# Kernel tuning notes

Hardware: AMD Instinct MI355X
Metric: run time of the kernel (lower is better)

## Reference

```python
import jax, jax.numpy as jnp
import numpy as np

BINS = 256
MIN_V = -0.25
MAX_V = 1.25
XSIGMA = 1.0 / float(np.sqrt(2.0 * np.pi))
DELTA = (MAX_V - MIN_V) / BINS
SIGMA = DELTA * XSIGMA
# constant prefactor applied once to the joint kernel: delta / (sqrt(2*pi)*sigma)
COEF = float(DELTA / (np.sqrt(2.0 * np.pi) * SIGMA))

B, N = 8, 32768


def setup_inputs() -> dict:
    key = jax.random.key(0)
    k1, k2, k3 = jax.random.split(key, 3)
    x1 = jax.random.uniform(k1, (B, N), dtype=jnp.float32)
    x2 = jax.random.uniform(k2, (B, N), dtype=jnp.float32)
    mask = jax.random.uniform(k3, (B, N), dtype=jnp.float32)
    return {"x1": x1, "x2": x2, "mask": mask}


def reference(x1, x2, mask):
    # bin centers: (bins,)
    centers = MIN_V + DELTA * (jnp.arange(BINS, dtype=x1.dtype) + 0.5)
    inv_s = 1.0 / SIGMA
    # Separable factorization of exp(-0.5*((x1-ci)^2+(x2-cj)^2)/sigma^2):
    # g1: (b, bins, N), g2: (b, bins, N) with mask folded into g2.
    d1 = (x1[:, None, :] - centers[None, :, None]) * inv_s
    d2 = (x2[:, None, :] - centers[None, :, None]) * inv_s
    g1 = jnp.exp(-0.5 * d1 * d1)
    g2 = jnp.exp(-0.5 * d2 * d2) * mask[:, None, :]
    # contract over N via batched matmul -> (b, bins, bins)
    hist = jnp.einsum("bin,bjn->bij", g1, g2)
    return COEF * hist
```

## Files before the change

### kernel.cpp

```cpp
#include <hip/hip_runtime.h>


#define BINS   256
#define NPTS   32768
#define BATCH  8
#define TROWS  8
#define NTILE  (BINS / TROWS)
#define WORDS  64

static constexpr float kInvDelta = 256.0f / 1.5f;
static constexpr float kUAdd     = 0.25f * (256.0f / 1.5f) - 0.5f;
static constexpr float kPi       = 3.14159265358979323846f;
static constexpr float kFix      = 1024.0f;
static constexpr float kInvFix   = 1.0f / 1024.0f;

__global__ __launch_bounds__(1024) void gh_gather(
    const float* __restrict__ x1, const float* __restrict__ x2,
    const float* __restrict__ mask, float* __restrict__ out)
{
    __shared__ unsigned long long tile[2 * TROWS * WORDS];
    const int tid = threadIdx.x;
    const int r0  = blockIdx.x * TROWS;
    const int b   = blockIdx.y;

    tile[tid] = 0ULL;
    __syncthreads();

    const float4* X1 = (const float4*)(x1   + b * NPTS);
    const float4* X2 = (const float4*)(x2   + b * NPTS);
    const float4* M  = (const float4*)(mask + b * NPTS);

#pragma unroll 2
    for (int it = 0; it < NPTS / 4096; ++it) {
        const int n4 = it * 1024 + tid;
        const float4 a4 = X1[n4];
        const float4 b4 = X2[n4];
        const float4 m4 = M[n4];

        const float pv1[4] = {a4.x, a4.y, a4.z, a4.w};
        const float pv2[4] = {b4.x, b4.y, b4.z, b4.w};
        const float pm[4]  = {m4.x, m4.y, m4.z, m4.w};

#pragma unroll
        for (int k = 0; k < 4; ++k) {
            const float u1 = fmaf(pv1[k], kInvDelta, kUAdd);
            const float u2 = fmaf(pv2[k], kInvDelta, kUAdd);
            const float fi = rintf(u1);
            const int   i0 = (int)fi;
            const float t1 = u1 - fi;

            int e = (((int)rintf(u2)) - 1) & ~1;
            e = min(250, max(0, e));
            const int  ph   = (e >> 1) & 1;
            const int  word = e >> 2;
            const float t2  = u2 - (float)e;

            float w1a[3];
#pragma unroll
            for (int a = 0; a < 3; ++a) {
                const float d = t1 - (float)(a - 1);
                w1a[a] = __expf(-kPi * d * d);
            }
            float W2[4];
#pragma unroll
            for (int c = 0; c < 4; ++c) {
                const float d = t2 - (float)c;
                W2[c] = __expf(-kPi * d * d) * (pm[k] * kFix);
            }

            const int rbase = i0 - 1 - r0;
            const int pbase = ph * (TROWS * WORDS) + word;
#pragma unroll
            for (int a = 0; a < 3; ++a) {
                const int r = rbase + a;
                if ((unsigned)r < TROWS) {
                    const float wa = w1a[a];
                    const unsigned f0 = (unsigned)fmaf(wa, W2[0], 0.5f);
                    const unsigned f1 = (unsigned)fmaf(wa, W2[1], 0.5f);
                    const unsigned f2 = (unsigned)fmaf(wa, W2[2], 0.5f);
                    const unsigned f3 = (unsigned)fmaf(wa, W2[3], 0.5f);
                    const unsigned long long w =
                        (unsigned long long)(f0 | (f1 << 16)) |
                        ((unsigned long long)(f2 | (f3 << 16)) << 32);
                    atomicAdd(&tile[pbase + r * WORDS], w);
                }
            }
        }
    }
    __syncthreads();

    {
        const int cell0 = tid * 2;
        const int r  = cell0 >> 8;
        const int c0 = cell0 & 255;
        float2 f2v;
        float* fp = &f2v.x;
#pragma unroll
        for (int i = 0; i < 2; ++i) {
            const int c = c0 + i;
            const unsigned long long we = tile[r * WORDS + (c >> 2)];
            unsigned v = (unsigned)(we >> (16 * (c & 3))) & 0xFFFFu;
            if (c >= 2) {
                const unsigned long long wo =
                    tile[TROWS * WORDS + r * WORDS + ((c - 2) >> 2)];
                v += (unsigned)(wo >> (16 * ((c - 2) & 3))) & 0xFFFFu;
            }
            fp[i] = (float)v * kInvFix;
        }
        float2* o2 = (float2*)(out + ((size_t)b * BINS + r0 + r) * BINS + c0);
        *o2 = f2v;
    }
}

extern "C" void kernel_launch(void* const* d_in, const int* in_sizes, int n_in,
                              void* d_out, int out_size, void* d_ws, size_t ws_size,
                              hipStream_t stream) {
    const float* x1   = (const float*)d_in[0];
    const float* x2   = (const float*)d_in[1];
    const float* mask = (const float*)d_in[2];
    float*       out  = (float*)d_out;

    gh_gather<<<dim3(NTILE, BATCH), 1024, 0, stream>>>(x1, x2, mask, out);
}
```

Before: 79.28 us.

## Split point range across blocks with workspace partial tiles and separate reduce kernel

Each block now handles a 16-row tile and a quarter of the points, giving 512 blocks of 512 threads instead of 256 blocks of 1024 threads. Partial fixed-point tiles go to workspace, and a second kernel sums the four chunks and unpacks them to float. This cuts the redundant per-block scan of all points (each block reads N/4 points for twice as many rows) and raises parallelism. The cost is a second launch, a workspace round-trip of about 8 MB, and possible 16-bit overflow is avoided by summing partials in 32-bit.

```diff
diff --git a/kernel.cpp b/kernel.cpp
--- a/kernel.cpp
+++ b/kernel.cpp
@@ -4,9 +4,12 @@
 #define BINS   256
 #define NPTS   32768
 #define BATCH  8
-#define TROWS  8
+#define TROWS  16
 #define NTILE  (BINS / TROWS)
+#define CHUNK  4
+#define PPC    (NPTS / CHUNK)
 #define WORDS  64
+#define TILE64 (2 * TROWS * WORDS)
 
 static constexpr float kInvDelta = 256.0f / 1.5f;
 static constexpr float kUAdd     = 0.25f * (256.0f / 1.5f) - 0.5f;
@@ -14,25 +17,28 @@
 static constexpr float kFix      = 1024.0f;
 static constexpr float kInvFix   = 1.0f / 1024.0f;
 
-__global__ __launch_bounds__(1024) void gh_gather(
+__global__ __launch_bounds__(512) void gh_part(
     const float* __restrict__ x1, const float* __restrict__ x2,
-    const float* __restrict__ mask, float* __restrict__ out)
+    const float* __restrict__ mask, unsigned long long* __restrict__ ws)
 {
-    __shared__ unsigned long long tile[2 * TROWS * WORDS];
+    __shared__ unsigned long long tile[TILE64];
     const int tid = threadIdx.x;
-    const int r0  = blockIdx.x * TROWS;
+    const int t   = blockIdx.x;
     const int b   = blockIdx.y;
+    const int z   = blockIdx.z;
+    const int r0  = t * TROWS;
 
-    tile[tid] = 0ULL;
+#pragma unroll
+    for (int i = tid; i < TILE64; i += 512) tile[i] = 0ULL;
     __syncthreads();
 
-    const float4* X1 = (const float4*)(x1   + b * NPTS);
-    const float4* X2 = (const float4*)(x2   + b * NPTS);
-    const float4* M  = (const float4*)(mask + b * NPTS);
+    const float4* X1 = (const float4*)(x1   + b * NPTS + z * PPC);
+    const float4* X2 = (const float4*)(x2   + b * NPTS + z * PPC);
+    const float4* M  = (const float4*)(mask + b * NPTS + z * PPC);
 
 #pragma unroll 2
-    for (int it = 0; it < NPTS / 4096; ++it) {
-        const int n4 = it * 1024 + tid;
+    for (int it = 0; it < PPC / 2048; ++it) {
+        const int n4 = it * 512 + tid;
         const float4 a4 = X1[n4];
         const float4 b4 = X2[n4];
         const float4 m4 = M[n4];
@@ -89,27 +95,42 @@
     }
     __syncthreads();
 
-    {
-        const int cell0 = tid * 2;
-        const int r  = cell0 >> 8;
-        const int c0 = cell0 & 255;
-        float2 f2v;
-        float* fp = &f2v.x;
+    unsigned long long* W = ws + (size_t)((b * NTILE + t) * CHUNK + z) * TILE64;
 #pragma unroll
-        for (int i = 0; i < 2; ++i) {
-            const int c = c0 + i;
-            const unsigned long long we = tile[r * WORDS + (c >> 2)];
-            unsigned v = (unsigned)(we >> (16 * (c & 3))) & 0xFFFFu;
-            if (c >= 2) {
-                const unsigned long long wo =
-                    tile[TROWS * WORDS + r * WORDS + ((c - 2) >> 2)];
-                v += (unsigned)(wo >> (16 * ((c - 2) & 3))) & 0xFFFFu;
-            }
-            fp[i] = (float)v * kInvFix;
+    for (int i = tid; i < TILE64; i += 512) W[i] = tile[i];
+}
+
+__global__ __launch_bounds__(1024) void gh_reduce(
+    const unsigned long long* __restrict__ ws, float* __restrict__ out)
+{
+    const int g     = blockIdx.x * 1024 + threadIdx.x;
+    const int cell0 = g * 2;
+    const int b     = cell0 >> 16;
+    const int rem   = cell0 & 65535;
+    const int r     = rem >> 8;
+    const int c0    = rem & 255;
+    const int t     = r >> 4;
+    const int rr    = r & 15;
+
+    const unsigned long long* W = ws + (size_t)((b * NTILE + t) * CHUNK) * TILE64;
+    unsigned a0 = 0, a1 = 0;
+#pragma unroll
+    for (int z = 0; z < CHUNK; ++z) {
+        const unsigned long long* Z = W + z * TILE64;
+        const unsigned long long we = Z[rr * WORDS + (c0 >> 2)];
+        a0 += (unsigned)(we >> (16 * (c0 & 3)))       & 0xFFFFu;
+        a1 += (unsigned)(we >> (16 * ((c0 + 1) & 3))) & 0xFFFFu;
+        if (c0 >= 2) {
+            const unsigned long long wo =
+                Z[TROWS * WORDS + rr * WORDS + ((c0 - 2) >> 2)];
+            a0 += (unsigned)(wo >> (16 * ((c0 - 2) & 3))) & 0xFFFFu;
+            a1 += (unsigned)(wo >> (16 * ((c0 - 1) & 3))) & 0xFFFFu;
         }
-        float2* o2 = (float2*)(out + ((size_t)b * BINS + r0 + r) * BINS + c0);
-        *o2 = f2v;
     }
+    float2 f;
+    f.x = (float)a0 * kInvFix;
+    f.y = (float)a1 * kInvFix;
+    *(float2*)(out + (size_t)cell0) = f;
 }
 
 extern "C" void kernel_launch(void* const* d_in, const int* in_sizes, int n_in,
@@ -119,6 +140,8 @@
     const float* x2   = (const float*)d_in[1];
     const float* mask = (const float*)d_in[2];
     float*       out  = (float*)d_out;
+    unsigned long long* ws = (unsigned long long*)d_ws;
 
-    gh_gather<<<dim3(NTILE, BATCH), 1024, 0, stream>>>(x1, x2, mask, out);
+    gh_part<<<dim3(NTILE, BATCH, CHUNK), 512, 0, stream>>>(x1, x2, mask, ws);
+    gh_reduce<<<dim3(BATCH * BINS * BINS / 2048), 1024, 0, stream>>>(ws, out);
 }
```

Measured after the change: 75.38 us. -4.9%, faster.
